# Performance work log

Measured on AMD Instinct MI355X. Metric: run time of the kernel, lower is better.

Reference implementation:

```python
import jax, jax.numpy as jnp
import numpy as np

N = 262144
D = 512
H = 512
G = 1024


def setup_inputs() -> dict:
    key = jax.random.key(0)
    k1, k2, k3, k4 = jax.random.split(key, 4)
    embed = jax.random.normal(k1, (N, D), dtype=jnp.float32)
    batch_index = jnp.sort(jax.random.randint(k2, (N,), 0, G)).astype(jnp.int64)
    # nn.Linear weights: W_att [atten_hidden, embed_size], V_att [1, atten_hidden]
    W_att = jax.random.normal(k3, (H, D), dtype=jnp.float32) * (1.0 / np.sqrt(D))
    V_att = jax.random.normal(k4, (1, H), dtype=jnp.float32) * (1.0 / np.sqrt(H))
    return {"embed": embed, "batch_index": batch_index, "W_att": W_att, "V_att": V_att, "num_segments": G}


def reference(embed, batch_index, W_att, V_att, num_segments):
    # beta = V(tanh(W(embed))).squeeze(-1)  -> [N]
    beta = jnp.einsum('nh,oh->no', jnp.tanh(jnp.einsum('nd,hd->nh', embed, W_att)), V_att).squeeze(-1)
    # segment softmax (unnormalized exp, as in the original module)
    exp_beta = jnp.exp(beta)
    grouped_sum = jax.ops.segment_sum(exp_beta, batch_index, num_segments=num_segments)  # [G]
    alpha = exp_beta / grouped_sum[batch_index]  # [N]
    # scatter-weighted sum of node embeddings per graph -> [G, D]
    result = jax.ops.segment_sum(alpha[:, None] * embed, batch_index, num_segments=num_segments)
    return result
```

## Files before the change

kernel.cpp:

```cpp
#include <hip/hip_runtime.h>
#include <hip/hip_bf16.h>

#define D_DIM 512
#define H_DIM 512
#define G_SEG 1024
#define BM    64
#define TILES 8

typedef __attribute__((ext_vector_type(8))) short bf16x8;
typedef __attribute__((ext_vector_type(4))) float f32x4;
typedef unsigned int u32;
typedef unsigned short u16;

#define WS_S   0
#define WS_WB  8192

#define BUF0_OFF  0
#define BUF1_OFF  (BM * 1024)
#define BETA_OFF  (2 * BM * 1024)
#define EBS_OFF   (BETA_OFF + 4 * BM * 4)
#define SIDX_OFF  (EBS_OFF + BM * 4)
#define SCR_OFF   (SIDX_OFF + BM * 4)
#define LDS_TOTAL (SCR_OFF + 4 * 512 * 4)

static __device__ __forceinline__ u16 f2bf(float f) {
    __hip_bfloat16 h = __float2bfloat16(f);
    return *(u16*)&h;
}
static __device__ __forceinline__ float bf2f(u16 u) {
    return __uint_as_float(((u32)u) << 16);
}
static __device__ __forceinline__ float fast_tanh(float x) {
    float e = exp2f(x * 2.885390081777927f);
    return 1.0f - 2.0f * __builtin_amdgcn_rcpf(e + 1.0f);
}
static __device__ __forceinline__ void barrier_lds() {
    asm volatile("s_waitcnt lgkmcnt(0)" ::: "memory");
    __builtin_amdgcn_s_barrier();
    __builtin_amdgcn_sched_barrier(0);
}

__global__ __launch_bounds__(256)
void cvt_w(const float* __restrict__ W, u16* __restrict__ Wb) {
    int t   = blockIdx.x * 256 + threadIdx.x;
    int lhi = t & 3;
    int c   = (t >> 2) & 511;
    int k32 = t >> 11;
    const float* src = W + (size_t)c * 512 + k32 * 32 + lhi * 8;
    float4 f0 = *(const float4*)(src);
    float4 f1 = *(const float4*)(src + 4);
    u16 h[8];
    h[0]=f2bf(f0.x); h[1]=f2bf(f0.y); h[2]=f2bf(f0.z); h[3]=f2bf(f0.w);
    h[4]=f2bf(f1.x); h[5]=f2bf(f1.y); h[6]=f2bf(f1.z); h[7]=f2bf(f1.w);
    *(uint4*)(Wb + (size_t)t * 8) = *(uint4*)h;
}

__global__ __launch_bounds__(256, 1)
void fused(const float* __restrict__ E, const int* __restrict__ BI,
           const u16* __restrict__ Wb, const float* __restrict__ V,
           float* __restrict__ out, float* __restrict__ S)
{
    extern __shared__ char smem[];
    const int tid = threadIdx.x;
    const int l   = tid & 63;
    const int w   = tid >> 6;
    const int l15 = l & 15;
    const int lhi = l >> 4;
    const int tile0 = blockIdx.x * TILES;

    const int bOffBase = ((w * 128 + l15) * 4 + lhi) * 16;
    const char* Wbb = (const char*)Wb;

    float4 LA[8], LB[8];
    auto issueB = [&](int gTile, int p, float4* L) {
        const float* Eb = E + (size_t)gTile * (BM * 512);
#pragma unroll
        for (int i = 0; i < 8; ++i) {
            int row  = w * 16 + p * 4 + (i >> 1);
            int half = i & 1;
            L[i] = *(const float4*)(Eb + (size_t)row * 512 + half * 256 + l * 4);
        }
    };
    auto writeB = [&](char* buf, int p, float4* L) {
#pragma unroll
        for (int i = 0; i < 8; ++i) {
            int row  = w * 16 + p * 4 + (i >> 1);
            int half = i & 1;
            int g16  = half * 32 + (l >> 1);
            int byte = row * 1024 + ((g16 * 16) ^ ((row & 7) << 4)) + (l & 1) * 8;
            u16 h[4];
            h[0] = f2bf(L[i].x); h[1] = f2bf(L[i].y);
            h[2] = f2bf(L[i].z); h[3] = f2bf(L[i].w);
            *(uint2*)(buf + byte) = *(uint2*)h;
        }
    };

    issueB(tile0, 0, LA);
    issueB(tile0, 1, LB);
    writeB(smem + BUF0_OFF, 0, LA);
    issueB(tile0, 2, LA);
    writeB(smem + BUF0_OFF, 1, LB);
    issueB(tile0, 3, LB);
    writeB(smem + BUF0_OFF, 2, LA);
    writeB(smem + BUF0_OFF, 3, LB);
    barrier_lds();

    bf16x8 bA[8], bB[8];
#pragma unroll
    for (int n = 0; n < 8; ++n)
        bA[n] = *(const bf16x8*)(Wbb + bOffBase + n * 1024);

    int cur = 0;
#pragma unroll 1
    for (int t = 0; t < TILES; ++t) {
        char* bufC = smem + (cur ? BUF1_OFF : BUF0_OFF);
        char* bufN = smem + (cur ? BUF0_OFF : BUF1_OFF);
        const bool more  = (t + 1 < TILES);
        const int  tNext = tile0 + t + 1;
        const int  nodeBase = (tile0 + t) * BM;

        f32x4 acc[4][8];
#pragma unroll
        for (int m = 0; m < 4; ++m)
#pragma unroll
            for (int n = 0; n < 8; ++n) acc[m][n] = (f32x4){0.f, 0.f, 0.f, 0.f};

#pragma unroll 1
        for (int kk2 = 0; kk2 < 8; ++kk2) {
            if (more && kk2 == 0) issueB(tNext, 0, LA);
            if (more && kk2 == 2) issueB(tNext, 1, LB);
            if (more && kk2 == 5) writeB(bufN, 0, LA);
            if (more && kk2 == 7) writeB(bufN, 1, LB);
            {
                const char* Wn = Wbb + ((size_t)(2 * kk2 + 1) << 15);
#pragma unroll
                for (int n = 0; n < 8; ++n)
                    bB[n] = *(const bf16x8*)(Wn + bOffBase + n * 1024);
                bf16x8 a[4];
                const int kbyte = (2 * kk2) * 64 + lhi * 16;
#pragma unroll
                for (int m = 0; m < 4; ++m) {
                    int row = m * 16 + l15;
                    a[m] = *(const bf16x8*)(bufC + row * 1024 + (kbyte ^ ((row & 7) << 4)));
                }
#pragma unroll
                for (int m = 0; m < 4; ++m)
#pragma unroll
                    for (int n = 0; n < 8; ++n)
                        acc[m][n] = __builtin_amdgcn_mfma_f32_16x16x32_bf16(a[m], bA[n], acc[m][n], 0, 0, 0);
            }
            {
                if (kk2 < 7) {
                    const char* Wn = Wbb + ((size_t)(2 * kk2 + 2) << 15);
#pragma unroll
                    for (int n = 0; n < 8; ++n)
                        bA[n] = *(const bf16x8*)(Wn + bOffBase + n * 1024);
                }
                bf16x8 a[4];
                const int kbyte = (2 * kk2 + 1) * 64 + lhi * 16;
#pragma unroll
                for (int m = 0; m < 4; ++m) {
                    int row = m * 16 + l15;
                    a[m] = *(const bf16x8*)(bufC + row * 1024 + (kbyte ^ ((row & 7) << 4)));
                }
#pragma unroll
                for (int m = 0; m < 4; ++m)
#pragma unroll
                    for (int n = 0; n < 8; ++n)
                        acc[m][n] = __builtin_amdgcn_mfma_f32_16x16x32_bf16(a[m], bB[n], acc[m][n], 0, 0, 0);
            }
        }

        if (more) issueB(tNext, 2, LA);
        if (more) {
#pragma unroll
            for (int n = 0; n < 8; ++n)
                bA[n] = *(const bf16x8*)(Wbb + bOffBase + n * 1024);
        }

        float Vv[8];
#pragma unroll
        for (int n = 0; n < 8; ++n)
            Vv[n] = V[w * 128 + n * 16 + l15];

        float bsum[4][4];
#pragma unroll
        for (int m = 0; m < 4; ++m)
#pragma unroll
            for (int r = 0; r < 4; ++r) {
                float s = 0.f;
#pragma unroll
                for (int n = 0; n < 8; ++n)
                    s += Vv[n] * fast_tanh(acc[m][n][r]);
                bsum[m][r] = s;
            }
#pragma unroll
        for (int off = 1; off <= 8; off <<= 1)
#pragma unroll
            for (int m = 0; m < 4; ++m)
#pragma unroll
                for (int r = 0; r < 4; ++r)
                    bsum[m][r] += __shfl_xor(bsum[m][r], off, 64);

        if (more) writeB(bufN, 2, LA);

        float* betaP = (float*)(smem + BETA_OFF);
        if (l15 == 0) {
#pragma unroll
            for (int m = 0; m < 4; ++m)
#pragma unroll
                for (int r = 0; r < 4; ++r)
                    betaP[w * BM + m * 16 + lhi * 4 + r] = bsum[m][r];
        }
        barrier_lds();

        if (more) issueB(tNext, 3, LB);

        float* ebs  = (float*)(smem + EBS_OFF);
        int*   sidx = (int*)(smem + SIDX_OFF);
        if (tid < BM) {
            float beta = betaP[tid] + betaP[BM + tid] + betaP[2 * BM + tid] + betaP[3 * BM + tid];
            float eb = expf(beta);
            ebs[tid] = eb;
            int g = BI[nodeBase + tid];
            sidx[tid] = g;
            int g0 = __shfl(g, 0, 64);
            if (__all(g == g0)) {
                float s = eb;
#pragma unroll
                for (int off = 1; off <= 32; off <<= 1)
                    s += __shfl_xor(s, off, 64);
                if (l == 0) atomicAdd(&S[g], s);
            } else {
                atomicAdd(&S[g], eb);
            }
        }
        barrier_lds();

        {
            float* scr = (float*)(smem + SCR_OFF) + w * 512;
            const int rbase = w * 16;
            float a8[8];
#pragma unroll
            for (int j = 0; j < 8; ++j) a8[j] = 0.f;
            int gcur = sidx[rbase];

#pragma unroll 1
            for (int rr = 0; rr < 16; ++rr) {
                int r = rbase + rr;
                int g = sidx[r];
                if (g != gcur) {
                    *(float4*)(scr + l * 8)     = make_float4(a8[0], a8[1], a8[2], a8[3]);
                    *(float4*)(scr + l * 8 + 4) = make_float4(a8[4], a8[5], a8[6], a8[7]);
                    asm volatile("s_waitcnt lgkmcnt(0)" ::: "memory");
#pragma unroll
                    for (int j = 0; j < 8; ++j)
                        atomicAdd(&out[(size_t)gcur * 512 + j * 64 + l], scr[j * 64 + l]);
#pragma unroll
                    for (int j = 0; j < 8; ++j) a8[j] = 0.f;
                    gcur = g;
                }
                float wgt = ebs[r];
                bf16x8 v = *(const bf16x8*)(bufC + r * 1024 + ((l * 16) ^ ((r & 7) << 4)));
#pragma unroll
                for (int j = 0; j < 8; ++j)
                    a8[j] += wgt * bf2f((u16)v[j]);
            }
            *(float4*)(scr + l * 8)     = make_float4(a8[0], a8[1], a8[2], a8[3]);
            *(float4*)(scr + l * 8 + 4) = make_float4(a8[4], a8[5], a8[6], a8[7]);
            asm volatile("s_waitcnt lgkmcnt(0)" ::: "memory");
#pragma unroll
            for (int j = 0; j < 8; ++j)
                atomicAdd(&out[(size_t)gcur * 512 + j * 64 + l], scr[j * 64 + l]);
        }

        if (more) writeB(bufN, 3, LB);
        barrier_lds();
        cur ^= 1;
    }
}

__global__ __launch_bounds__(256)
void finalize_kernel(float* __restrict__ out, const float* __restrict__ S) {
    int idx = blockIdx.x * 256 + threadIdx.x;
    float s = S[idx >> 9];
    float v = out[idx];
    out[idx] = (s != 0.f) ? v * __builtin_amdgcn_rcpf(s) : 0.f;
}

extern "C" void kernel_launch(void* const* d_in, const int* in_sizes, int n_in,
                              void* d_out, int out_size, void* d_ws, size_t ws_size,
                              hipStream_t stream) {
    const float* E  = (const float*)d_in[0];
    const int*   BI = (const int*)d_in[1];
    const float* W  = (const float*)d_in[2];
    const float* V  = (const float*)d_in[3];
    float* out = (float*)d_out;
    char*  ws  = (char*)d_ws;
    const int Ntot = in_sizes[0] / D_DIM;

    float* S  = (float*)(ws + WS_S);
    u16*   Wb = (u16*)(ws + WS_WB);

    hipMemsetAsync(S, 0, G_SEG * 4, stream);
    hipMemsetAsync(out, 0, (size_t)out_size * 4, stream);
    hipFuncSetAttribute((const void*)fused,
                        hipFuncAttributeMaxDynamicSharedMemorySize, LDS_TOTAL);

    cvt_w<<<128, 256, 0, stream>>>(W, Wb);
    fused<<<Ntot / (BM * TILES), 256, LDS_TOTAL, stream>>>(E, BI, Wb, V, out, S);
    finalize_kernel<<<out_size / 256, 256, 0, stream>>>(out, S);
}
```

Measured before the change: 346.9 us.

## Pre-convert embeddings to swizzled bf16 and stream tiles via direct global-to-LDS loads

Adds a separate kernel that converts the fp32 embeddings into a bf16 copy stored in the swizzled tile layout. The fused kernel then loads each tile straight into LDS with global_load_lds, double-buffered one tile ahead, instead of loading fp32 into registers, converting and writing to LDS. TILES per block doubles and V loads are hoisted out of the tile loop. The cost is an extra full pass over the fp32 input (read 512MB, write 256MB) in exchange for halved fused-kernel reads and freed VGPRs and VALU work.

```diff
diff --git a/kernel.cpp b/kernel.cpp
--- a/kernel.cpp
+++ b/kernel.cpp
@@ -5,15 +5,16 @@
 #define H_DIM 512
 #define G_SEG 1024
 #define BM    64
-#define TILES 8
+#define TILES 16
 
 typedef __attribute__((ext_vector_type(8))) short bf16x8;
 typedef __attribute__((ext_vector_type(4))) float f32x4;
 typedef unsigned int u32;
 typedef unsigned short u16;
 
-#define WS_S   0
-#define WS_WB  8192
+#define WS_S    0
+#define WS_WB   8192
+#define WS_E16  (1u << 20)
 
 #define BUF0_OFF  0
 #define BUF1_OFF  (BM * 1024)
@@ -23,6 +24,12 @@
 #define SCR_OFF   (SIDX_OFF + BM * 4)
 #define LDS_TOTAL (SCR_OFF + 4 * 512 * 4)
 
+#define GLOBAL_AS __attribute__((address_space(1)))
+#define LDS_AS    __attribute__((address_space(3)))
+
+static __device__ __forceinline__ void gload_lds16(const void* g, void* l) {
+    __builtin_amdgcn_global_load_lds((const GLOBAL_AS u32*)g, (LDS_AS u32*)l, 16, 0, 0);
+}
 static __device__ __forceinline__ u16 f2bf(float f) {
     __hip_bfloat16 h = __float2bfloat16(f);
     return *(u16*)&h;
@@ -33,6 +40,12 @@
 static __device__ __forceinline__ float fast_tanh(float x) {
     float e = exp2f(x * 2.885390081777927f);
     return 1.0f - 2.0f * __builtin_amdgcn_rcpf(e + 1.0f);
+}
+static __device__ __forceinline__ void pack8(const float4& a, const float4& b, void* dst) {
+    u16 h[8];
+    h[0]=f2bf(a.x); h[1]=f2bf(a.y); h[2]=f2bf(a.z); h[3]=f2bf(a.w);
+    h[4]=f2bf(b.x); h[5]=f2bf(b.y); h[6]=f2bf(b.z); h[7]=f2bf(b.w);
+    *(uint4*)dst = *(uint4*)h;
 }
 static __device__ __forceinline__ void barrier_lds() {
     asm volatile("s_waitcnt lgkmcnt(0)" ::: "memory");
@@ -47,16 +60,26 @@
     int c   = (t >> 2) & 511;
     int k32 = t >> 11;
     const float* src = W + (size_t)c * 512 + k32 * 32 + lhi * 8;
-    float4 f0 = *(const float4*)(src);
-    float4 f1 = *(const float4*)(src + 4);
-    u16 h[8];
-    h[0]=f2bf(f0.x); h[1]=f2bf(f0.y); h[2]=f2bf(f0.z); h[3]=f2bf(f0.w);
-    h[4]=f2bf(f1.x); h[5]=f2bf(f1.y); h[6]=f2bf(f1.z); h[7]=f2bf(f1.w);
-    *(uint4*)(Wb + (size_t)t * 8) = *(uint4*)h;
+    pack8(*(const float4*)src, *(const float4*)(src + 4), Wb + (size_t)t * 8);
+}
+
+__global__ __launch_bounds__(256)
+void cvt_e(const float* __restrict__ E, u16* __restrict__ E16, int nChunks) {
+    const int stride = gridDim.x * 256;
+#pragma unroll 1
+    for (int c = blockIdx.x * 256 + threadIdx.x; c < nChunks; c += stride) {
+        int rowg = c >> 6, j = c & 63;
+        const float* src = E + (size_t)rowg * 512 + j * 8;
+        float4 f0 = *(const float4*)src;
+        float4 f1 = *(const float4*)(src + 4);
+        int tau = rowg >> 6, r = rowg & 63;
+        size_t off = ((size_t)tau << 16) + r * 1024 + ((j << 4) ^ ((r & 7) << 4));
+        pack8(f0, f1, (char*)E16 + off);
+    }
 }
 
 __global__ __launch_bounds__(256, 1)
-void fused(const float* __restrict__ E, const int* __restrict__ BI,
+void fused(const u16* __restrict__ E16, const int* __restrict__ BI,
            const u16* __restrict__ Wb, const float* __restrict__ V,
            float* __restrict__ out, float* __restrict__ S)
 {
@@ -71,39 +94,21 @@
     const int bOffBase = ((w * 128 + l15) * 4 + lhi) * 16;
     const char* Wbb = (const char*)Wb;
 
-    float4 LA[8], LB[8];
-    auto issueB = [&](int gTile, int p, float4* L) {
-        const float* Eb = E + (size_t)gTile * (BM * 512);
-#pragma unroll
-        for (int i = 0; i < 8; ++i) {
-            int row  = w * 16 + p * 4 + (i >> 1);
-            int half = i & 1;
-            L[i] = *(const float4*)(Eb + (size_t)row * 512 + half * 256 + l * 4);
-        }
+    float Vv[8];
+#pragma unroll
+    for (int n = 0; n < 8; ++n)
+        Vv[n] = V[w * 128 + n * 16 + l15];
+
+    auto issueTile = [&](int gTile, char* buf) {
+        const char* src = (const char*)E16 + ((size_t)gTile << 16)
+                        + (size_t)w * 16384 + (size_t)l * 16;
+        char* dst = buf + w * 16384;
+#pragma unroll
+        for (int i = 0; i < 16; ++i)
+            gload_lds16(src + i * 1024, dst + i * 1024);
     };
-    auto writeB = [&](char* buf, int p, float4* L) {
-#pragma unroll
-        for (int i = 0; i < 8; ++i) {
-            int row  = w * 16 + p * 4 + (i >> 1);
-            int half = i & 1;
-            int g16  = half * 32 + (l >> 1);
-            int byte = row * 1024 + ((g16 * 16) ^ ((row & 7) << 4)) + (l & 1) * 8;
-            u16 h[4];
-            h[0] = f2bf(L[i].x); h[1] = f2bf(L[i].y);
-            h[2] = f2bf(L[i].z); h[3] = f2bf(L[i].w);
-            *(uint2*)(buf + byte) = *(uint2*)h;
-        }
-    };
-
-    issueB(tile0, 0, LA);
-    issueB(tile0, 1, LB);
-    writeB(smem + BUF0_OFF, 0, LA);
-    issueB(tile0, 2, LA);
-    writeB(smem + BUF0_OFF, 1, LB);
-    issueB(tile0, 3, LB);
-    writeB(smem + BUF0_OFF, 2, LA);
-    writeB(smem + BUF0_OFF, 3, LB);
-    barrier_lds();
+
+    issueTile(tile0, smem + BUF0_OFF);
 
     bf16x8 bA[8], bB[8];
 #pragma unroll
@@ -115,9 +120,18 @@
     for (int t = 0; t < TILES; ++t) {
         char* bufC = smem + (cur ? BUF1_OFF : BUF0_OFF);
         char* bufN = smem + (cur ? BUF0_OFF : BUF1_OFF);
-        const bool more  = (t + 1 < TILES);
-        const int  tNext = tile0 + t + 1;
+        const bool more = (t + 1 < TILES);
         const int  nodeBase = (tile0 + t) * BM;
+
+        if (more) {
+            issueTile(tile0 + t + 1, bufN);
+            asm volatile("s_waitcnt vmcnt(16)" ::: "memory");
+        } else {
+            asm volatile("s_waitcnt vmcnt(0)" ::: "memory");
+        }
+        __builtin_amdgcn_sched_barrier(0);
+        __builtin_amdgcn_s_barrier();
+        __builtin_amdgcn_sched_barrier(0);
 
         f32x4 acc[4][8];
 #pragma unroll
@@ -127,10 +141,6 @@
 
 #pragma unroll 1
         for (int kk2 = 0; kk2 < 8; ++kk2) {
-            if (more && kk2 == 0) issueB(tNext, 0, LA);
-            if (more && kk2 == 2) issueB(tNext, 1, LB);
-            if (more && kk2 == 5) writeB(bufN, 0, LA);
-            if (more && kk2 == 7) writeB(bufN, 1, LB);
             {
                 const char* Wn = Wbb + ((size_t)(2 * kk2 + 1) << 15);
 #pragma unroll
@@ -171,17 +181,11 @@
             }
         }
 
-        if (more) issueB(tNext, 2, LA);
         if (more) {
 #pragma unroll
             for (int n = 0; n < 8; ++n)
                 bA[n] = *(const bf16x8*)(Wbb + bOffBase + n * 1024);
         }
-
-        float Vv[8];
-#pragma unroll
-        for (int n = 0; n < 8; ++n)
-            Vv[n] = V[w * 128 + n * 16 + l15];
 
         float bsum[4][4];
 #pragma unroll
@@ -202,8 +206,6 @@
                 for (int r = 0; r < 4; ++r)
                     bsum[m][r] += __shfl_xor(bsum[m][r], off, 64);
 
-        if (more) writeB(bufN, 2, LA);
-
         float* betaP = (float*)(smem + BETA_OFF);
         if (l15 == 0) {
 #pragma unroll
@@ -213,8 +215,6 @@
                     betaP[w * BM + m * 16 + lhi * 4 + r] = bsum[m][r];
         }
         barrier_lds();
-
-        if (more) issueB(tNext, 3, LB);
 
         float* ebs  = (float*)(smem + EBS_OFF);
         int*   sidx = (int*)(smem + SIDX_OFF);
@@ -274,8 +274,8 @@
                 atomicAdd(&out[(size_t)gcur * 512 + j * 64 + l], scr[j * 64 + l]);
         }
 
-        if (more) writeB(bufN, 3, LB);
-        barrier_lds();
+        __builtin_amdgcn_s_barrier();
+        __builtin_amdgcn_sched_barrier(0);
         cur ^= 1;
     }
 }
@@ -299,8 +299,9 @@
     char*  ws  = (char*)d_ws;
     const int Ntot = in_sizes[0] / D_DIM;
 
-    float* S  = (float*)(ws + WS_S);
-    u16*   Wb = (u16*)(ws + WS_WB);
+    float* S   = (float*)(ws + WS_S);
+    u16*   Wb  = (u16*)(ws + WS_WB);
+    u16*   E16 = (u16*)(ws + WS_E16);
 
     hipMemsetAsync(S, 0, G_SEG * 4, stream);
     hipMemsetAsync(out, 0, (size_t)out_size * 4, stream);
@@ -308,6 +309,7 @@
                         hipFuncAttributeMaxDynamicSharedMemorySize, LDS_TOTAL);
 
     cvt_w<<<128, 256, 0, stream>>>(W, Wb);
-    fused<<<Ntot / (BM * TILES), 256, LDS_TOTAL, stream>>>(E, BI, Wb, V, out, S);
+    cvt_e<<<2048, 256, 0, stream>>>(E, E16, Ntot * 64);
+    fused<<<Ntot / (BM * TILES), 256, LDS_TOTAL, stream>>>(E16, BI, Wb, V, out, S);
     finalize_kernel<<<out_size / 256, 256, 0, stream>>>(out, S);
 }
```

After: 443.9 us. 1.28x slower.
